# Optimization experiments

Measured on AMD Instinct MI355X. Metric: run time of the kernel, lower is better.

## Reference

```python
import jax, jax.numpy as jnp
import numpy as np

N_NODES = 50000
N_EDGES = 600000
N_GRAPHS = 64
D_NODE = 64
D_EDGE = 16
HID = 128
N_LAYERS = 3
LN_EPS = 1e-5


def setup_inputs() -> dict:
    key = jax.random.key(0)
    ks = jax.random.split(key, 16)
    inp = {
        'x': jax.random.normal(ks[0], (N_NODES, D_NODE), dtype=jnp.float32),
        'edge_index': jax.random.randint(ks[1], (2, N_EDGES), 0, N_NODES, dtype=jnp.int64),
        'edge_attr': jax.random.normal(ks[2], (N_EDGES, D_EDGE), dtype=jnp.float32),
        'batch': jnp.sort(jax.random.randint(ks[3], (N_NODES,), 0, N_GRAPHS, dtype=jnp.int64)),
    }
    def lin(k, fan_in, fan_out):
        bound = 1.0 / np.sqrt(fan_in)
        kw, kb = jax.random.split(k)
        w = jax.random.uniform(kw, (fan_in, fan_out), minval=-bound, maxval=bound, dtype=jnp.float32)
        b = jax.random.uniform(kb, (fan_out,), minval=-bound, maxval=bound, dtype=jnp.float32)
        return w, b
    inp['enc_w'], inp['enc_b'] = lin(ks[4], D_NODE, HID)
    inp['ln_g'] = jnp.ones((HID,), jnp.float32)
    inp['ln_b'] = jnp.zeros((HID,), jnp.float32)
    inp['edge_w'], inp['edge_b'] = lin(ks[5], D_EDGE, HID // 2)
    cw, cb = [], []
    for i in range(N_LAYERS):
        w, b = lin(ks[6 + i], HID, HID)
        cw.append(w); cb.append(b)
    inp['conv_ws'] = jnp.stack(cw)  # [L, HID, HID]
    inp['conv_bs'] = jnp.stack(cb)  # [L, HID]
    inp['c1_w'], inp['c1_b'] = lin(ks[10], HID, HID // 2)
    inp['c2_w'], inp['c2_b'] = lin(ks[11], HID // 2, 1)
    return inp


def _layernorm(h, g, b):
    mu = jnp.mean(h, axis=-1, keepdims=True)
    var = jnp.mean(jnp.square(h - mu), axis=-1, keepdims=True)
    return (h - mu) * jax.lax.rsqrt(var + LN_EPS) * g + b


def _gcn_forward(x, edge_attr, batch, src, dst,
                 enc_w, enc_b, ln_g, ln_b, edge_w, edge_b,
                 conv_ws, conv_bs, c1_w, c1_b, c2_w, c2_b):
    # node encoder: Linear -> ReLU -> LayerNorm
    h = _layernorm(jax.nn.relu(x @ enc_w + enc_b), ln_g, ln_b)
    # edge encoder (output unused downstream, kept for fidelity)
    _ = jax.nn.relu(edge_attr @ edge_w + edge_b)
    # GCN normalization with self-loops: deg = in-degree + 1
    deg = jax.ops.segment_sum(jnp.ones((src.shape[0],), h.dtype), dst, num_segments=N_NODES) + 1.0
    dis = jax.lax.rsqrt(deg)  # deg >= 1
    edge_norm = (dis[src] * dis[dst])[:, None]
    self_norm = (dis * dis)[:, None]  # 1/deg for self-loop
    for i in range(N_LAYERS):
        hw = h @ conv_ws[i]
        agg = jax.ops.segment_sum(hw[src] * edge_norm, dst, num_segments=N_NODES)
        h = agg + hw * self_norm + conv_bs[i]
        h = jax.nn.relu(h)  # dropout is identity at eval
    # global mean pool over graphs
    sums = jax.ops.segment_sum(h, batch, num_segments=N_GRAPHS)
    cnts = jax.ops.segment_sum(jnp.ones((h.shape[0],), h.dtype), batch, num_segments=N_GRAPHS)
    pooled = sums / jnp.maximum(cnts, 1.0)[:, None]
    # classifier: Linear -> ReLU -> (Dropout) -> Linear
    return jax.nn.relu(pooled @ c1_w + c1_b) @ c2_w + c2_b


def reference(x, edge_index, edge_attr, batch, enc_w, enc_b, ln_g, ln_b,
              edge_w, edge_b, conv_ws, conv_bs, c1_w, c1_b, c2_w, c2_b):
    src, dst = edge_index[0], edge_index[1]
    return _gcn_forward(x, edge_attr, batch, src, dst, enc_w, enc_b, ln_g, ln_b,
                        edge_w, edge_b, conv_ws, conv_bs, c1_w, c1_b, c2_w, c2_b)
```

## Files before the change

### kernel.cpp

```cpp
#include <hip/hip_runtime.h>

#define HID 128
#define DNODE 64
#define NNODES 50000
#define NEDGES 600000
#define NGRAPHS 64
#define LN_EPS 1e-5f
#define SCAN_BLK 256
#define NSCAN ((NNODES + SCAN_BLK - 1) / SCAN_BLK)

#define NZERO (NNODES + NGRAPHS * HID)
#define NZERO4 (NZERO / 4)
#define Z_BLKS ((NZERO4 + 255) / 256)
#define PKWC_BLKS (3 * 16384 / 256)
#define PKWE_BLKS (8192 / 256)
#define BND_BLKS ((NNODES + 255) / 256)

#define CNT_BLKS ((NEDGES + 255) / 256)
#define ENC_BLKS ((NNODES + 63) / 64)

#define CONV_BLKS ((NNODES + 63) / 64)
#define FILL_BLKS ((NEDGES + 255) / 256)

#define GC_BLKS (NNODES / 16)

typedef __attribute__((ext_vector_type(8))) short bf16x8;
typedef __attribute__((ext_vector_type(8))) unsigned short u16x8;
typedef __attribute__((ext_vector_type(4))) float f32x4;

static __device__ __forceinline__ unsigned short f2bf(float f) {
  unsigned int u = __float_as_uint(f);
  u += 0x7fffu + ((u >> 16) & 1u);
  return (unsigned short)(u >> 16);
}
static __device__ __forceinline__ float bf2f(unsigned short h) {
  return __uint_as_float(((unsigned int)h) << 16);
}

__global__ void __launch_bounds__(256) prep0_kernel(
    int4* __restrict__ zp, const float* __restrict__ W,
    unsigned short* __restrict__ Wp, const float* __restrict__ enc_w,
    unsigned short* __restrict__ Wpe, const int* __restrict__ batch,
    int* __restrict__ gstart, int* __restrict__ gend) {
  int b = blockIdx.x;
  if (b < Z_BLKS) {
    int i = b * 256 + threadIdx.x;
    if (i < NZERO4) zp[i] = make_int4(0, 0, 0, 0);
  } else if (b < Z_BLKS + PKWC_BLKS) {
    int t = (b - Z_BLKS) * 256 + threadIdx.x;
    int i = t & 7;
    int lane = (t >> 3) & 63;
    int kk = (t >> 9) & 3;
    int nt = (t >> 11) & 7;
    int layer = t >> 14;
    int k = kk * 32 + (lane >> 4) * 8 + i;
    int n = nt * 16 + (lane & 15);
    Wp[t] = f2bf(W[((size_t)layer * HID + k) * HID + n]);
  } else if (b < Z_BLKS + PKWC_BLKS + PKWE_BLKS) {
    int t = (b - Z_BLKS - PKWC_BLKS) * 256 + threadIdx.x;
    int i = t & 7;
    int lane = (t >> 3) & 63;
    int kk = (t >> 9) & 1;
    int nt = (t >> 10) & 7;
    int k = kk * 32 + (lane >> 4) * 8 + i;
    int n = nt * 16 + (lane & 15);
    Wpe[t] = f2bf(enc_w[(size_t)k * HID + n]);
  } else {
    int i = (b - Z_BLKS - PKWC_BLKS - PKWE_BLKS) * 256 + threadIdx.x;
    if (i < NNODES) {
      int g = batch[i];
      if (i == 0 || batch[i - 1] != g) gstart[g] = i;
      if (i == NNODES - 1 || batch[i + 1] != g) gend[g] = i + 1;
    }
  }
}

__global__ void __launch_bounds__(256) prep1_kernel(
    const float* __restrict__ x, const unsigned short* __restrict__ Wpe,
    const float* __restrict__ enc_b, const float* __restrict__ ln_g,
    const float* __restrict__ ln_b, unsigned short* __restrict__ Abf,
    const int* __restrict__ dst, int* __restrict__ degi,
    int* __restrict__ erank) {
  __shared__ __align__(16) unsigned short tile[4][16][136];
  int blk = blockIdx.x;
  if (blk < CNT_BLKS) {
    int e = blk * 256 + threadIdx.x;
    if (e < NEDGES) erank[e] = atomicAdd(&degi[dst[e]], 1);
    return;
  }
  int b2 = blk - CNT_BLKS;
  int wave = threadIdx.x >> 6;
  int lane = threadIdx.x & 63;
  int l15 = lane & 15, h = lane >> 4;
  int base = b2 * 64 + wave * 16;
  int row = base + l15;
  int rowc = row < NNODES ? row : NNODES - 1;
  const float* xr = x + (size_t)rowc * DNODE;
  bf16x8 a[2];
#pragma unroll
  for (int kk = 0; kk < 2; ++kk) {
    float4 p0 = *(const float4*)(xr + kk * 32 + h * 8);
    float4 p1 = *(const float4*)(xr + kk * 32 + h * 8 + 4);
    a[kk][0] = (short)f2bf(p0.x); a[kk][1] = (short)f2bf(p0.y);
    a[kk][2] = (short)f2bf(p0.z); a[kk][3] = (short)f2bf(p0.w);
    a[kk][4] = (short)f2bf(p1.x); a[kk][5] = (short)f2bf(p1.y);
    a[kk][6] = (short)f2bf(p1.z); a[kk][7] = (short)f2bf(p1.w);
  }
  f32x4 acc[8];
#pragma unroll
  for (int nt = 0; nt < 8; ++nt) acc[nt] = (f32x4)(0.f);
  const bf16x8* wp = (const bf16x8*)Wpe;
#pragma unroll
  for (int kk = 0; kk < 2; ++kk)
#pragma unroll
    for (int nt = 0; nt < 8; ++nt)
      acc[nt] = __builtin_amdgcn_mfma_f32_16x16x32_bf16(a[kk], wp[(nt * 2 + kk) * 64 + lane],
                                                        acc[nt], 0, 0, 0);
  float s[4] = {0.f, 0.f, 0.f, 0.f}, s2[4] = {0.f, 0.f, 0.f, 0.f};
#pragma unroll
  for (int nt = 0; nt < 8; ++nt) {
    float bcol = enc_b[nt * 16 + l15];
#pragma unroll
    for (int r = 0; r < 4; ++r) {
      float v = fmaxf(acc[nt][r] + bcol, 0.f);
      acc[nt][r] = v;
      s[r] += v;
      s2[r] = fmaf(v, v, s2[r]);
    }
  }
#pragma unroll
  for (int r = 0; r < 4; ++r) {
#pragma unroll
    for (int o = 1; o < 16; o <<= 1) {
      s[r] += __shfl_xor(s[r], o);
      s2[r] += __shfl_xor(s2[r], o);
    }
  }
  float mu[4], rstd[4];
#pragma unroll
  for (int r = 0; r < 4; ++r) {
    mu[r] = s[r] * (1.0f / HID);
    float var = s2[r] * (1.0f / HID) - mu[r] * mu[r];
    rstd[r] = rsqrtf(var + LN_EPS);
  }
#pragma unroll
  for (int nt = 0; nt < 8; ++nt) {
    float gcol = ln_g[nt * 16 + l15], bbcol = ln_b[nt * 16 + l15];
#pragma unroll
    for (int r = 0; r < 4; ++r)
      tile[wave][h * 4 + r][nt * 16 + l15] =
          f2bf((acc[nt][r] - mu[r]) * rstd[r] * gcol + bbcol);
  }
  __syncthreads();
  int trow = lane >> 2, tseg = lane & 3;
  int orow = base + trow;
  if (orow < NNODES) {
#pragma unroll
    for (int q = 0; q < 4; ++q) {
      u16x8 v = *(const u16x8*)&tile[wave][trow][tseg * 32 + q * 8];
      *(u16x8*)(Abf + (size_t)orow * HID + tseg * 32 + q * 8) = v;
    }
  }
}

__global__ void __launch_bounds__(SCAN_BLK) blocksum_kernel(
    const int* __restrict__ degi, int* __restrict__ bsum) {
  int i = blockIdx.x * SCAN_BLK + threadIdx.x;
  int v = (i < NNODES) ? degi[i] : 0;
#pragma unroll
  for (int off = 32; off; off >>= 1) v += __shfl_down(v, off);
  __shared__ int wsum[4];
  if ((threadIdx.x & 63) == 0) wsum[threadIdx.x >> 6] = v;
  __syncthreads();
  if (threadIdx.x == 0) bsum[blockIdx.x] = wsum[0] + wsum[1] + wsum[2] + wsum[3];
}

__global__ void __launch_bounds__(SCAN_BLK) offsets_kernel(
    const int* __restrict__ degi, const int* __restrict__ bsum,
    int* __restrict__ off, float* __restrict__ dis) {
  int b = blockIdx.x, t = threadIdx.x;
  __shared__ int sb[SCAN_BLK];
  __shared__ int s[SCAN_BLK];
  __shared__ int wred[4];
  sb[t] = (t < NSCAN) ? bsum[t] : 0;
  __syncthreads();
  int v = (t < b) ? sb[t] : 0;
#pragma unroll
  for (int o = 32; o; o >>= 1) v += __shfl_down(v, o);
  if ((t & 63) == 0) wred[t >> 6] = v;
  __syncthreads();
  int base = wred[0] + wred[1] + wred[2] + wred[3];
  int i = b * SCAN_BLK + t;
  int dv = (i < NNODES) ? degi[i] : 0;
  s[t] = dv;
  __syncthreads();
  for (int d = 1; d < SCAN_BLK; d <<= 1) {
    int x = (t >= d) ? s[t - d] : 0;
    __syncthreads();
    s[t] += x;
    __syncthreads();
  }
  if (i < NNODES) {
    int excl = s[t] - dv + base;
    off[i] = excl;
    dis[i] = rsqrtf((float)dv + 1.0f);
  }
  if (b == 0 && t == 0) off[NNODES] = NEDGES;
}

__global__ void __launch_bounds__(256) fillconv_kernel(
    const unsigned short* __restrict__ Abf, const unsigned short* __restrict__ Wp,
    unsigned short* __restrict__ Bbf, const int* __restrict__ src,
    const int* __restrict__ dst, const int* __restrict__ erank,
    const int* __restrict__ off, const float* __restrict__ dis,
    unsigned int* __restrict__ epack) {
  __shared__ __align__(16) unsigned short tile[4][16][136];
  int blk = blockIdx.x;
  if (blk >= CONV_BLKS) {
    int e = (blk - CONV_BLKS) * 256 + threadIdx.x;
    if (e >= NEDGES) return;
    int d = dst[e];
    int sN = src[e];
    int r = erank[e];
    epack[off[d] + r] =
        ((unsigned int)f2bf(dis[sN] * dis[d]) << 16) | (unsigned int)sN;
    return;
  }
  int wave = threadIdx.x >> 6;
  int lane = threadIdx.x & 63;
  int base = blk * 64 + wave * 16;
  int l15 = lane & 15, hi = lane >> 4;
  int row = base + l15;
  int rowc = row < NNODES ? row : NNODES - 1;
  bf16x8 a[4];
#pragma unroll
  for (int kk = 0; kk < 4; ++kk)
    a[kk] = *(const bf16x8*)(Abf + (size_t)rowc * HID + kk * 32 + hi * 8);
  f32x4 acc[8];
#pragma unroll
  for (int nt = 0; nt < 8; ++nt) acc[nt] = (f32x4)(0.f);
#pragma unroll
  for (int kk = 0; kk < 4; ++kk) {
#pragma unroll
    for (int nt = 0; nt < 8; ++nt) {
      bf16x8 w = *(const bf16x8*)(Wp + (((nt * 4 + kk) * 64 + lane) << 3));
      acc[nt] = __builtin_amdgcn_mfma_f32_16x16x32_bf16(a[kk], w, acc[nt], 0, 0, 0);
    }
  }
#pragma unroll
  for (int nt = 0; nt < 8; ++nt)
#pragma unroll
    for (int r = 0; r < 4; ++r)
      tile[wave][hi * 4 + r][nt * 16 + l15] = f2bf(acc[nt][r]);
  __syncthreads();
  int trow = lane >> 2, tseg = lane & 3;
  int orow = base + trow;
  if (orow < NNODES) {
#pragma unroll
    for (int s = 0; s < 4; ++s) {
      u16x8 v = *(const u16x8*)&tile[wave][trow][tseg * 32 + s * 8];
      *(u16x8*)(Bbf + (size_t)orow * HID + tseg * 32 + s * 8) = v;
    }
  }
}

__global__ void __launch_bounds__(1024) gc_kernel(
    const int* __restrict__ off, const unsigned int* __restrict__ epack,
    const float* __restrict__ dis, const float* __restrict__ bias,
    const unsigned short* __restrict__ Bin, const unsigned short* __restrict__ Wnext,
    unsigned short* __restrict__ Bout) {
  __shared__ __align__(16) unsigned short As[16][136];
  __shared__ __align__(16) unsigned short Bs[16][136];
  int w = threadIdx.x >> 6, lane = threadIdx.x & 63;
  int n = blockIdx.x * 16 + w;
  int slot = lane >> 4, p = lane & 15;
  int lo = off[n], hi = off[n + 1];
  float acc0[8], acc1[8];
#pragma unroll
  for (int i = 0; i < 8; ++i) { acc0[i] = 0.f; acc1[i] = 0.f; }
  int idx = lo + slot;
  for (; idx + 4 < hi; idx += 8) {
    unsigned int e0 = epack[idx];
    unsigned int e1 = epack[idx + 4];
    float w0 = bf2f((unsigned short)(e0 >> 16));
    float w1 = bf2f((unsigned short)(e1 >> 16));
    u16x8 v0 = *(const u16x8*)(Bin + (size_t)(e0 & 0xFFFFu) * HID + p * 8);
    u16x8 v1 = *(const u16x8*)(Bin + (size_t)(e1 & 0xFFFFu) * HID + p * 8);
#pragma unroll
    for (int i = 0; i < 8; ++i) acc0[i] = fmaf(bf2f(v0[i]), w0, acc0[i]);
#pragma unroll
    for (int i = 0; i < 8; ++i) acc1[i] = fmaf(bf2f(v1[i]), w1, acc1[i]);
  }
  if (idx < hi) {
    unsigned int e0 = epack[idx];
    float w0 = bf2f((unsigned short)(e0 >> 16));
    u16x8 v0 = *(const u16x8*)(Bin + (size_t)(e0 & 0xFFFFu) * HID + p * 8);
#pragma unroll
    for (int i = 0; i < 8; ++i) acc0[i] = fmaf(bf2f(v0[i]), w0, acc0[i]);
  }
#pragma unroll
  for (int i = 0; i < 8; ++i) {
    float a = acc0[i] + acc1[i];
    a += __shfl_xor(a, 16);
    a += __shfl_xor(a, 32);
    acc0[i] = a;
  }
  if (slot == 0) {
    float dn = dis[n];
    float d2 = dn * dn;
    u16x8 selfv = *(const u16x8*)(Bin + (size_t)n * HID + p * 8);
    float4 b0 = ((const float4*)bias)[p * 2];
    float4 b1 = ((const float4*)bias)[p * 2 + 1];
    float bb[8] = {b0.x, b0.y, b0.z, b0.w, b1.x, b1.y, b1.z, b1.w};
    u16x8 o;
#pragma unroll
    for (int i = 0; i < 8; ++i) {
      float v = fmaxf(fmaf(bf2f(selfv[i]), d2, bb[i]) + acc0[i], 0.f);
      o[i] = f2bf(v);
    }
    *(u16x8*)&As[w][p * 8] = o;
  }
  __syncthreads();
  if (w < 8) {
    bf16x8 a[4];
#pragma unroll
    for (int kk = 0; kk < 4; ++kk)
      a[kk] = *(const bf16x8*)&As[p][kk * 32 + slot * 8];
    f32x4 acc = (f32x4)(0.f);
#pragma unroll
    for (int kk = 0; kk < 4; ++kk) {
      bf16x8 wf = *(const bf16x8*)(Wnext + (((w * 4 + kk) * 64 + lane) << 3));
      acc = __builtin_amdgcn_mfma_f32_16x16x32_bf16(a[kk], wf, acc, 0, 0, 0);
    }
#pragma unroll
    for (int r = 0; r < 4; ++r)
      Bs[slot * 4 + r][w * 16 + p] = f2bf(acc[r]);
  }
  __syncthreads();
  if (threadIdx.x < 256) {
    int row = threadIdx.x >> 4, seg = threadIdx.x & 15;
    *(u16x8*)(Bout + (size_t)(blockIdx.x * 16 + row) * HID + seg * 8) =
        *(const u16x8*)&Bs[row][seg * 8];
  }
}

__global__ void __launch_bounds__(1024) g2pool_kernel(
    const int* __restrict__ off, const unsigned int* __restrict__ epack,
    const float* __restrict__ dis, const float* __restrict__ bias,
    const unsigned short* __restrict__ Bin, const int* __restrict__ batch,
    float* __restrict__ sums) {
  __shared__ float Ps[16][132];
  __shared__ int bg[16];
  int w = threadIdx.x >> 6, lane = threadIdx.x & 63;
  int n = blockIdx.x * 16 + w;
  int slot = lane >> 4, p = lane & 15;
  int lo = off[n], hi = off[n + 1];
  float acc0[8], acc1[8];
#pragma unroll
  for (int i = 0; i < 8; ++i) { acc0[i] = 0.f; acc1[i] = 0.f; }
  int idx = lo + slot;
  for (; idx + 4 < hi; idx += 8) {
    unsigned int e0 = epack[idx];
    unsigned int e1 = epack[idx + 4];
    float w0 = bf2f((unsigned short)(e0 >> 16));
    float w1 = bf2f((unsigned short)(e1 >> 16));
    u16x8 v0 = *(const u16x8*)(Bin + (size_t)(e0 & 0xFFFFu) * HID + p * 8);
    u16x8 v1 = *(const u16x8*)(Bin + (size_t)(e1 & 0xFFFFu) * HID + p * 8);
#pragma unroll
    for (int i = 0; i < 8; ++i) acc0[i] = fmaf(bf2f(v0[i]), w0, acc0[i]);
#pragma unroll
    for (int i = 0; i < 8; ++i) acc1[i] = fmaf(bf2f(v1[i]), w1, acc1[i]);
  }
  if (idx < hi) {
    unsigned int e0 = epack[idx];
    float w0 = bf2f((unsigned short)(e0 >> 16));
    u16x8 v0 = *(const u16x8*)(Bin + (size_t)(e0 & 0xFFFFu) * HID + p * 8);
#pragma unroll
    for (int i = 0; i < 8; ++i) acc0[i] = fmaf(bf2f(v0[i]), w0, acc0[i]);
  }
#pragma unroll
  for (int i = 0; i < 8; ++i) {
    float a = acc0[i] + acc1[i];
    a += __shfl_xor(a, 16);
    a += __shfl_xor(a, 32);
    acc0[i] = a;
  }
  if (slot == 0) {
    float dn = dis[n];
    float d2 = dn * dn;
    u16x8 selfv = *(const u16x8*)(Bin + (size_t)n * HID + p * 8);
    float4 b0 = ((const float4*)bias)[p * 2];
    float4 b1 = ((const float4*)bias)[p * 2 + 1];
    float bb[8] = {b0.x, b0.y, b0.z, b0.w, b1.x, b1.y, b1.z, b1.w};
    float4 o0, o1;
    o0.x = fmaxf(fmaf(bf2f(selfv[0]), d2, bb[0]) + acc0[0], 0.f);
    o0.y = fmaxf(fmaf(bf2f(selfv[1]), d2, bb[1]) + acc0[1], 0.f);
    o0.z = fmaxf(fmaf(bf2f(selfv[2]), d2, bb[2]) + acc0[2], 0.f);
    o0.w = fmaxf(fmaf(bf2f(selfv[3]), d2, bb[3]) + acc0[3], 0.f);
    o1.x = fmaxf(fmaf(bf2f(selfv[4]), d2, bb[4]) + acc0[4], 0.f);
    o1.y = fmaxf(fmaf(bf2f(selfv[5]), d2, bb[5]) + acc0[5], 0.f);
    o1.z = fmaxf(fmaf(bf2f(selfv[6]), d2, bb[6]) + acc0[6], 0.f);
    o1.w = fmaxf(fmaf(bf2f(selfv[7]), d2, bb[7]) + acc0[7], 0.f);
    *(float4*)&Ps[w][p * 8] = o0;
    *(float4*)&Ps[w][p * 8 + 4] = o1;
  }
  if (threadIdx.x < 16) bg[threadIdx.x] = batch[blockIdx.x * 16 + threadIdx.x];
  __syncthreads();
  if (threadIdx.x < HID) {
    int j = threadIdx.x;
    float a = 0.f;
    int cur = bg[0];
    for (int r = 0; r < 16; ++r) {
      int g = bg[r];
      if (g != cur) { atomicAdd(&sums[cur * HID + j], a); a = 0.f; cur = g; }
      a += Ps[r][j];
    }
    atomicAdd(&sums[cur * HID + j], a);
  }
}

__global__ void __launch_bounds__(64) cls_kernel(
    const float* __restrict__ sums, const int* __restrict__ gstart,
    const int* __restrict__ gend, const float* __restrict__ c1w,
    const float* __restrict__ c1b, const float* __restrict__ c2w,
    const float* __restrict__ c2b, float* __restrict__ out) {
  int g = blockIdx.x;
  int j = threadIdx.x;
  __shared__ float pooled[HID];
  float cnt = (float)(gend[g] - gstart[g]);
  float inv = 1.0f / fmaxf(cnt, 1.0f);
  pooled[j] = sums[g * HID + j] * inv;
  pooled[j + 64] = sums[g * HID + j + 64] * inv;
  __syncthreads();
  float s = c1b[j];
#pragma unroll 8
  for (int k = 0; k < HID; ++k) s = fmaf(pooled[k], c1w[k * 64 + j], s);
  s = fmaxf(s, 0.f) * c2w[j];
#pragma unroll
  for (int off = 32; off; off >>= 1) s += __shfl_down(s, off);
  if (j == 0) out[g] = s + c2b[0];
}

extern "C" void kernel_launch(void* const* d_in, const int* in_sizes, int n_in,
                              void* d_out, int out_size, void* d_ws, size_t ws_size,
                              hipStream_t stream) {
  const float* x = (const float*)d_in[0];
  const int* edge_index = (const int*)d_in[1];
  const int* batch = (const int*)d_in[3];
  const float* enc_w = (const float*)d_in[4];
  const float* enc_b = (const float*)d_in[5];
  const float* ln_g = (const float*)d_in[6];
  const float* ln_b = (const float*)d_in[7];
  const float* conv_ws = (const float*)d_in[10];
  const float* conv_bs = (const float*)d_in[11];
  const float* c1w = (const float*)d_in[12];
  const float* c1b = (const float*)d_in[13];
  const float* c2w = (const float*)d_in[14];
  const float* c2b = (const float*)d_in[15];
  float* out = (float*)d_out;

  unsigned short* Abf = (unsigned short*)d_ws;
  unsigned short* B1 = Abf + (size_t)NNODES * HID;
  unsigned short* B2 = B1 + (size_t)NNODES * HID;
  unsigned short* Wp = B2 + (size_t)NNODES * HID;
  unsigned short* Wpe = Wp + 3 * 16384;
  unsigned int* epack = (unsigned int*)(Wpe + 8192);
  int* erank = (int*)(epack + NEDGES);
  int* degi = erank + NEDGES;
  float* sums = (float*)(degi + NNODES);
  int* off = (int*)(sums + NGRAPHS * HID);
  float* dis = (float*)(off + NNODES + 1);
  int* bsum = (int*)(dis + NNODES);
  int* gstart = bsum + SCAN_BLK;
  int* gend = gstart + NGRAPHS;

  const int* srcp = edge_index;
  const int* dstp = edge_index + NEDGES;

  prep0_kernel<<<Z_BLKS + PKWC_BLKS + PKWE_BLKS + BND_BLKS, 256, 0, stream>>>(
      (int4*)degi, conv_ws, Wp, enc_w, Wpe, batch, gstart, gend);
  prep1_kernel<<<CNT_BLKS + ENC_BLKS, 256, 0, stream>>>(
      x, Wpe, enc_b, ln_g, ln_b, Abf, dstp, degi, erank);
  blocksum_kernel<<<NSCAN, SCAN_BLK, 0, stream>>>(degi, bsum);
  offsets_kernel<<<NSCAN, SCAN_BLK, 0, stream>>>(degi, bsum, off, dis);
  fillconv_kernel<<<CONV_BLKS + FILL_BLKS, 256, 0, stream>>>(
      Abf, Wp, B1, srcp, dstp, erank, off, dis, epack);

  gc_kernel<<<GC_BLKS, 1024, 0, stream>>>(off, epack, dis, conv_bs, B1,
                                          Wp + (size_t)1 * 16384, B2);
  gc_kernel<<<GC_BLKS, 1024, 0, stream>>>(off, epack, dis, conv_bs + HID, B2,
                                          Wp + (size_t)2 * 16384, B1);
  g2pool_kernel<<<GC_BLKS, 1024, 0, stream>>>(off, epack, dis, conv_bs + 2 * HID,
                                              B1, batch, sums);
  cls_kernel<<<NGRAPHS, 64, 0, stream>>>(sums, gstart, gend, c1w, c1b, c2w, c2b, out);
}
```

Measured before the change: 182.5 us.

## Store node features as FP8 and fuse first conv GEMM into encoder

The hidden-feature buffers between layers are now stored as FP8 (e4m3) instead of bf16. This halves the bytes gathered per edge in the aggregation kernels and the bytes written per layer. The first conv matmul is also fused into the encoder kernel, which removes the Abf intermediate and the separate conv pass from the fill kernel. The trade is extra conversion instructions and a notable loss of precision in the activations, which may hurt accuracy tolerance.

Result: faster. 167.9 us (-8.0%).

```diff
diff --git a/kernel.cpp b/kernel.cpp
--- a/kernel.cpp
+++ b/kernel.cpp
@@ -18,8 +18,6 @@
 
 #define CNT_BLKS ((NEDGES + 255) / 256)
 #define ENC_BLKS ((NNODES + 63) / 64)
-
-#define CONV_BLKS ((NNODES + 63) / 64)
 #define FILL_BLKS ((NEDGES + 255) / 256)
 
 #define GC_BLKS (NNODES / 16)
@@ -27,6 +25,7 @@
 typedef __attribute__((ext_vector_type(8))) short bf16x8;
 typedef __attribute__((ext_vector_type(8))) unsigned short u16x8;
 typedef __attribute__((ext_vector_type(4))) float f32x4;
+typedef __attribute__((ext_vector_type(2))) float f32x2;
 
 static __device__ __forceinline__ unsigned short f2bf(float f) {
   unsigned int u = __float_as_uint(f);
@@ -35,6 +34,17 @@
 }
 static __device__ __forceinline__ float bf2f(unsigned short h) {
   return __uint_as_float(((unsigned int)h) << 16);
+}
+static __device__ __forceinline__ void fp8x4_to_f32(unsigned int w, float* o) {
+  f32x2 lo = __builtin_amdgcn_cvt_pk_f32_fp8(w, false);
+  f32x2 hi = __builtin_amdgcn_cvt_pk_f32_fp8(w, true);
+  o[0] = lo[0]; o[1] = lo[1]; o[2] = hi[0]; o[3] = hi[1];
+}
+static __device__ __forceinline__ unsigned int f32x4_to_fp8(float a, float b,
+                                                            float c, float d) {
+  unsigned int v = __builtin_amdgcn_cvt_pk_fp8_f32(a, b, 0, false);
+  v = __builtin_amdgcn_cvt_pk_fp8_f32(c, d, v, true);
+  return v;
 }
 
 __global__ void __launch_bounds__(256) prep0_kernel(
@@ -77,10 +87,10 @@
 
 __global__ void __launch_bounds__(256) prep1_kernel(
     const float* __restrict__ x, const unsigned short* __restrict__ Wpe,
-    const float* __restrict__ enc_b, const float* __restrict__ ln_g,
-    const float* __restrict__ ln_b, unsigned short* __restrict__ Abf,
-    const int* __restrict__ dst, int* __restrict__ degi,
-    int* __restrict__ erank) {
+    const unsigned short* __restrict__ Wp0, const float* __restrict__ enc_b,
+    const float* __restrict__ ln_g, const float* __restrict__ ln_b,
+    unsigned char* __restrict__ B1, const int* __restrict__ dst,
+    int* __restrict__ degi, int* __restrict__ erank) {
   __shared__ __align__(16) unsigned short tile[4][16][136];
   int blk = blockIdx.x;
   if (blk < CNT_BLKS) {
@@ -152,13 +162,40 @@
           f2bf((acc[nt][r] - mu[r]) * rstd[r] * gcol + bbcol);
   }
   __syncthreads();
+  bf16x8 a2[4];
+#pragma unroll
+  for (int kk = 0; kk < 4; ++kk)
+    a2[kk] = *(const bf16x8*)&tile[wave][l15][kk * 32 + h * 8];
+  __syncthreads();
+  f32x4 acc2[8];
+#pragma unroll
+  for (int nt = 0; nt < 8; ++nt) acc2[nt] = (f32x4)(0.f);
+#pragma unroll
+  for (int kk = 0; kk < 4; ++kk) {
+#pragma unroll
+    for (int nt = 0; nt < 8; ++nt) {
+      bf16x8 wf = *(const bf16x8*)(Wp0 + (((nt * 4 + kk) * 64 + lane) << 3));
+      acc2[nt] = __builtin_amdgcn_mfma_f32_16x16x32_bf16(a2[kk], wf, acc2[nt], 0, 0, 0);
+    }
+  }
+#pragma unroll
+  for (int nt = 0; nt < 8; ++nt)
+#pragma unroll
+    for (int r = 0; r < 4; ++r)
+      tile[wave][h * 4 + r][nt * 16 + l15] = f2bf(acc2[nt][r]);
+  __syncthreads();
   int trow = lane >> 2, tseg = lane & 3;
   int orow = base + trow;
   if (orow < NNODES) {
 #pragma unroll
     for (int q = 0; q < 4; ++q) {
       u16x8 v = *(const u16x8*)&tile[wave][trow][tseg * 32 + q * 8];
-      *(u16x8*)(Abf + (size_t)orow * HID + tseg * 32 + q * 8) = v;
+      uint2 o;
+      o.x = f32x4_to_fp8(bf2f((unsigned short)v[0]), bf2f((unsigned short)v[1]),
+                         bf2f((unsigned short)v[2]), bf2f((unsigned short)v[3]));
+      o.y = f32x4_to_fp8(bf2f((unsigned short)v[4]), bf2f((unsigned short)v[5]),
+                         bf2f((unsigned short)v[6]), bf2f((unsigned short)v[7]));
+      *(uint2*)(B1 + (size_t)orow * HID + tseg * 32 + q * 8) = o;
     }
   }
 }
@@ -208,67 +245,24 @@
   if (b == 0 && t == 0) off[NNODES] = NEDGES;
 }
 
-__global__ void __launch_bounds__(256) fillconv_kernel(
-    const unsigned short* __restrict__ Abf, const unsigned short* __restrict__ Wp,
-    unsigned short* __restrict__ Bbf, const int* __restrict__ src,
-    const int* __restrict__ dst, const int* __restrict__ erank,
-    const int* __restrict__ off, const float* __restrict__ dis,
-    unsigned int* __restrict__ epack) {
-  __shared__ __align__(16) unsigned short tile[4][16][136];
-  int blk = blockIdx.x;
-  if (blk >= CONV_BLKS) {
-    int e = (blk - CONV_BLKS) * 256 + threadIdx.x;
-    if (e >= NEDGES) return;
-    int d = dst[e];
-    int sN = src[e];
-    int r = erank[e];
-    epack[off[d] + r] =
-        ((unsigned int)f2bf(dis[sN] * dis[d]) << 16) | (unsigned int)sN;
-    return;
-  }
-  int wave = threadIdx.x >> 6;
-  int lane = threadIdx.x & 63;
-  int base = blk * 64 + wave * 16;
-  int l15 = lane & 15, hi = lane >> 4;
-  int row = base + l15;
-  int rowc = row < NNODES ? row : NNODES - 1;
-  bf16x8 a[4];
-#pragma unroll
-  for (int kk = 0; kk < 4; ++kk)
-    a[kk] = *(const bf16x8*)(Abf + (size_t)rowc * HID + kk * 32 + hi * 8);
-  f32x4 acc[8];
-#pragma unroll
-  for (int nt = 0; nt < 8; ++nt) acc[nt] = (f32x4)(0.f);
-#pragma unroll
-  for (int kk = 0; kk < 4; ++kk) {
-#pragma unroll
-    for (int nt = 0; nt < 8; ++nt) {
-      bf16x8 w = *(const bf16x8*)(Wp + (((nt * 4 + kk) * 64 + lane) << 3));
-      acc[nt] = __builtin_amdgcn_mfma_f32_16x16x32_bf16(a[kk], w, acc[nt], 0, 0, 0);
-    }
-  }
-#pragma unroll
-  for (int nt = 0; nt < 8; ++nt)
-#pragma unroll
-    for (int r = 0; r < 4; ++r)
-      tile[wave][hi * 4 + r][nt * 16 + l15] = f2bf(acc[nt][r]);
-  __syncthreads();
-  int trow = lane >> 2, tseg = lane & 3;
-  int orow = base + trow;
-  if (orow < NNODES) {
-#pragma unroll
-    for (int s = 0; s < 4; ++s) {
-      u16x8 v = *(const u16x8*)&tile[wave][trow][tseg * 32 + s * 8];
-      *(u16x8*)(Bbf + (size_t)orow * HID + tseg * 32 + s * 8) = v;
-    }
-  }
+__global__ void __launch_bounds__(256) fill_kernel(
+    const int* __restrict__ src, const int* __restrict__ dst,
+    const int* __restrict__ erank, const int* __restrict__ off,
+    const float* __restrict__ dis, unsigned int* __restrict__ epack) {
+  int e = blockIdx.x * 256 + threadIdx.x;
+  if (e >= NEDGES) return;
+  int d = dst[e];
+  int sN = src[e];
+  int r = erank[e];
+  epack[off[d] + r] =
+      ((unsigned int)f2bf(dis[sN] * dis[d]) << 16) | (unsigned int)sN;
 }
 
 __global__ void __launch_bounds__(1024) gc_kernel(
     const int* __restrict__ off, const unsigned int* __restrict__ epack,
     const float* __restrict__ dis, const float* __restrict__ bias,
-    const unsigned short* __restrict__ Bin, const unsigned short* __restrict__ Wnext,
-    unsigned short* __restrict__ Bout) {
+    const unsigned char* __restrict__ Bin, const unsigned short* __restrict__ Wnext,
+    unsigned char* __restrict__ Bout) {
   __shared__ __align__(16) unsigned short As[16][136];
   __shared__ __align__(16) unsigned short Bs[16][136];
   int w = threadIdx.x >> 6, lane = threadIdx.x & 63;
@@ -284,19 +278,24 @@
     unsigned int e1 = epack[idx + 4];
     float w0 = bf2f((unsigned short)(e0 >> 16));
     float w1 = bf2f((unsigned short)(e1 >> 16));
-    u16x8 v0 = *(const u16x8*)(Bin + (size_t)(e0 & 0xFFFFu) * HID + p * 8);
-    u16x8 v1 = *(const u16x8*)(Bin + (size_t)(e1 & 0xFFFFu) * HID + p * 8);
-#pragma unroll
-    for (int i = 0; i < 8; ++i) acc0[i] = fmaf(bf2f(v0[i]), w0, acc0[i]);
-#pragma unroll
-    for (int i = 0; i < 8; ++i) acc1[i] = fmaf(bf2f(v1[i]), w1, acc1[i]);
+    uint2 v0 = *(const uint2*)(Bin + (size_t)(e0 & 0xFFFFu) * HID + p * 8);
+    uint2 v1 = *(const uint2*)(Bin + (size_t)(e1 & 0xFFFFu) * HID + p * 8);
+    float f0[8], f1[8];
+    fp8x4_to_f32(v0.x, f0); fp8x4_to_f32(v0.y, f0 + 4);
+    fp8x4_to_f32(v1.x, f1); fp8x4_to_f32(v1.y, f1 + 4);
+#pragma unroll
+    for (int i = 0; i < 8; ++i) acc0[i] = fmaf(f0[i], w0, acc0[i]);
+#pragma unroll
+    for (int i = 0; i < 8; ++i) acc1[i] = fmaf(f1[i], w1, acc1[i]);
   }
   if (idx < hi) {
     unsigned int e0 = epack[idx];
     float w0 = bf2f((unsigned short)(e0 >> 16));
-    u16x8 v0 = *(const u16x8*)(Bin + (size_t)(e0 & 0xFFFFu) * HID + p * 8);
-#pragma unroll
-    for (int i = 0; i < 8; ++i) acc0[i] = fmaf(bf2f(v0[i]), w0, acc0[i]);
+    uint2 v0 = *(const uint2*)(Bin + (size_t)(e0 & 0xFFFFu) * HID + p * 8);
+    float f0[8];
+    fp8x4_to_f32(v0.x, f0); fp8x4_to_f32(v0.y, f0 + 4);
+#pragma unroll
+    for (int i = 0; i < 8; ++i) acc0[i] = fmaf(f0[i], w0, acc0[i]);
   }
 #pragma unroll
   for (int i = 0; i < 8; ++i) {
@@ -308,15 +307,17 @@
   if (slot == 0) {
     float dn = dis[n];
     float d2 = dn * dn;
-    u16x8 selfv = *(const u16x8*)(Bin + (size_t)n * HID + p * 8);
+    uint2 sv = *(const uint2*)(Bin + (size_t)n * HID + p * 8);
+    float sf[8];
+    fp8x4_to_f32(sv.x, sf); fp8x4_to_f32(sv.y, sf + 4);
     float4 b0 = ((const float4*)bias)[p * 2];
     float4 b1 = ((const float4*)bias)[p * 2 + 1];
     float bb[8] = {b0.x, b0.y, b0.z, b0.w, b1.x, b1.y, b1.z, b1.w};
     u16x8 o;
 #pragma unroll
     for (int i = 0; i < 8; ++i) {
-      float v = fmaxf(fmaf(bf2f(selfv[i]), d2, bb[i]) + acc0[i], 0.f);
-      o[i] = f2bf(v);
+      float v = fmaxf(fmaf(sf[i], d2, bb[i]) + acc0[i], 0.f);
+      o[i] = (short)f2bf(v);
     }
     *(u16x8*)&As[w][p * 8] = o;
   }
@@ -339,15 +340,20 @@
   __syncthreads();
   if (threadIdx.x < 256) {
     int row = threadIdx.x >> 4, seg = threadIdx.x & 15;
-    *(u16x8*)(Bout + (size_t)(blockIdx.x * 16 + row) * HID + seg * 8) =
-        *(const u16x8*)&Bs[row][seg * 8];
+    u16x8 v = *(const u16x8*)&Bs[row][seg * 8];
+    uint2 o;
+    o.x = f32x4_to_fp8(bf2f((unsigned short)v[0]), bf2f((unsigned short)v[1]),
+                       bf2f((unsigned short)v[2]), bf2f((unsigned short)v[3]));
+    o.y = f32x4_to_fp8(bf2f((unsigned short)v[4]), bf2f((unsigned short)v[5]),
+                       bf2f((unsigned short)v[6]), bf2f((unsigned short)v[7]));
+    *(uint2*)(Bout + (size_t)(blockIdx.x * 16 + row) * HID + seg * 8) = o;
   }
 }
 
 __global__ void __launch_bounds__(1024) g2pool_kernel(
     const int* __restrict__ off, const unsigned int* __restrict__ epack,
     const float* __restrict__ dis, const float* __restrict__ bias,
-    const unsigned short* __restrict__ Bin, const int* __restrict__ batch,
+    const unsigned char* __restrict__ Bin, const int* __restrict__ batch,
     float* __restrict__ sums) {
   __shared__ float Ps[16][132];
   __shared__ int bg[16];
@@ -364,19 +370,24 @@
     unsigned int e1 = epack[idx + 4];
     float w0 = bf2f((unsigned short)(e0 >> 16));
     float w1 = bf2f((unsigned short)(e1 >> 16));
-    u16x8 v0 = *(const u16x8*)(Bin + (size_t)(e0 & 0xFFFFu) * HID + p * 8);
-    u16x8 v1 = *(const u16x8*)(Bin + (size_t)(e1 & 0xFFFFu) * HID + p * 8);
-#pragma unroll
-    for (int i = 0; i < 8; ++i) acc0[i] = fmaf(bf2f(v0[i]), w0, acc0[i]);
-#pragma unroll
-    for (int i = 0; i < 8; ++i) acc1[i] = fmaf(bf2f(v1[i]), w1, acc1[i]);
+    uint2 v0 = *(const uint2*)(Bin + (size_t)(e0 & 0xFFFFu) * HID + p * 8);
+    uint2 v1 = *(const uint2*)(Bin + (size_t)(e1 & 0xFFFFu) * HID + p * 8);
+    float f0[8], f1[8];
+    fp8x4_to_f32(v0.x, f0); fp8x4_to_f32(v0.y, f0 + 4);
+    fp8x4_to_f32(v1.x, f1); fp8x4_to_f32(v1.y, f1 + 4);
+#pragma unroll
+    for (int i = 0; i < 8; ++i) acc0[i] = fmaf(f0[i], w0, acc0[i]);
+#pragma unroll
+    for (int i = 0; i < 8; ++i) acc1[i] = fmaf(f1[i], w1, acc1[i]);
   }
   if (idx < hi) {
     unsigned int e0 = epack[idx];
     float w0 = bf2f((unsigned short)(e0 >> 16));
-    u16x8 v0 = *(const u16x8*)(Bin + (size_t)(e0 & 0xFFFFu) * HID + p * 8);
-#pragma unroll
-    for (int i = 0; i < 8; ++i) acc0[i] = fmaf(bf2f(v0[i]), w0, acc0[i]);
+    uint2 v0 = *(const uint2*)(Bin + (size_t)(e0 & 0xFFFFu) * HID + p * 8);
+    float f0[8];
+    fp8x4_to_f32(v0.x, f0); fp8x4_to_f32(v0.y, f0 + 4);
+#pragma unroll
+    for (int i = 0; i < 8; ++i) acc0[i] = fmaf(f0[i], w0, acc0[i]);
   }
 #pragma unroll
   for (int i = 0; i < 8; ++i) {
@@ -388,19 +399,21 @@
   if (slot == 0) {
     float dn = dis[n];
     float d2 = dn * dn;
-    u16x8 selfv = *(const u16x8*)(Bin + (size_t)n * HID + p * 8);
+    uint2 sv = *(const uint2*)(Bin + (size_t)n * HID + p * 8);
+    float sf[8];
+    fp8x4_to_f32(sv.x, sf); fp8x4_to_f32(sv.y, sf + 4);
     float4 b0 = ((const float4*)bias)[p * 2];
     float4 b1 = ((const float4*)bias)[p * 2 + 1];
     float bb[8] = {b0.x, b0.y, b0.z, b0.w, b1.x, b1.y, b1.z, b1.w};
     float4 o0, o1;
-    o0.x = fmaxf(fmaf(bf2f(selfv[0]), d2, bb[0]) + acc0[0], 0.f);
-    o0.y = fmaxf(fmaf(bf2f(selfv[1]), d2, bb[1]) + acc0[1], 0.f);
-    o0.z = fmaxf(fmaf(bf2f(selfv[2]), d2, bb[2]) + acc0[2], 0.f);
-    o0.w = fmaxf(fmaf(bf2f(selfv[3]), d2, bb[3]) + acc0[3], 0.f);
-    o1.x = fmaxf(fmaf(bf2f(selfv[4]), d2, bb[4]) + acc0[4], 0.f);
-    o1.y = fmaxf(fmaf(bf2f(selfv[5]), d2, bb[5]) + acc0[5], 0.f);
-    o1.z = fmaxf(fmaf(bf2f(selfv[6]), d2, bb[6]) + acc0[6], 0.f);
-    o1.w = fmaxf(fmaf(bf2f(selfv[7]), d2, bb[7]) + acc0[7], 0.f);
+    o0.x = fmaxf(fmaf(sf[0], d2, bb[0]) + acc0[0], 0.f);
+    o0.y = fmaxf(fmaf(sf[1], d2, bb[1]) + acc0[1], 0.f);
+    o0.z = fmaxf(fmaf(sf[2], d2, bb[2]) + acc0[2], 0.f);
+    o0.w = fmaxf(fmaf(sf[3], d2, bb[3]) + acc0[3], 0.f);
+    o1.x = fmaxf(fmaf(sf[4], d2, bb[4]) + acc0[4], 0.f);
+    o1.y = fmaxf(fmaf(sf[5], d2, bb[5]) + acc0[5], 0.f);
+    o1.z = fmaxf(fmaf(sf[6], d2, bb[6]) + acc0[6], 0.f);
+    o1.w = fmaxf(fmaf(sf[7], d2, bb[7]) + acc0[7], 0.f);
     *(float4*)&Ps[w][p * 8] = o0;
     *(float4*)&Ps[w][p * 8 + 4] = o1;
   }
@@ -459,10 +472,9 @@
   const float* c2b = (const float*)d_in[15];
   float* out = (float*)d_out;
 
-  unsigned short* Abf = (unsigned short*)d_ws;
-  unsigned short* B1 = Abf + (size_t)NNODES * HID;
-  unsigned short* B2 = B1 + (size_t)NNODES * HID;
-  unsigned short* Wp = B2 + (size_t)NNODES * HID;
+  unsigned char* B1 = (unsigned char*)d_ws;
+  unsigned char* B2 = B1 + (size_t)NNODES * HID;
+  unsigned short* Wp = (unsigned short*)(B2 + (size_t)NNODES * HID);
   unsigned short* Wpe = Wp + 3 * 16384;
   unsigned int* epack = (unsigned int*)(Wpe + 8192);
   int* erank = (int*)(epack + NEDGES);
@@ -480,11 +492,10 @@
   prep0_kernel<<<Z_BLKS + PKWC_BLKS + PKWE_BLKS + BND_BLKS, 256, 0, stream>>>(
       (int4*)degi, conv_ws, Wp, enc_w, Wpe, batch, gstart, gend);
   prep1_kernel<<<CNT_BLKS + ENC_BLKS, 256, 0, stream>>>(
-      x, Wpe, enc_b, ln_g, ln_b, Abf, dstp, degi, erank);
+      x, Wpe, Wp, enc_b, ln_g, ln_b, B1, dstp, degi, erank);
   blocksum_kernel<<<NSCAN, SCAN_BLK, 0, stream>>>(degi, bsum);
   offsets_kernel<<<NSCAN, SCAN_BLK, 0, stream>>>(degi, bsum, off, dis);
-  fillconv_kernel<<<CONV_BLKS + FILL_BLKS, 256, 0, stream>>>(
-      Abf, Wp, B1, srcp, dstp, erank, off, dis, epack);
+  fill_kernel<<<FILL_BLKS, 256, 0, stream>>>(srcp, dstp, erank, off, dis, epack);
 
   gc_kernel<<<GC_BLKS, 1024, 0, stream>>>(off, epack, dis, conv_bs, B1,
                                           Wp + (size_t)1 * 16384, B2);
```
